# Performance work log

Measured on AMD Instinct MI355X. Metric: run time of the kernel, lower is better.

## Reference

```python
import jax, jax.numpy as jnp
import numpy as np

N = 50000          # nodes
E = 800000         # edges
F_IN = 128         # num_node_features
H = 64             # hidden_channels
G = 64             # graphs in batch
C = 10             # num_classes
L_HID = 3          # num_hidden_layers
EPS = 1e-5


def setup_inputs() -> dict:
    key = jax.random.key(0)
    ks = jax.random.split(key, 16)
    x = jax.random.normal(ks[0], (N, F_IN), dtype=jnp.float32)
    edge_index = jax.random.randint(ks[1], (2, E), 0, N, dtype=jnp.int32)
    batch = jnp.sort(jax.random.randint(ks[2], (N,), 0, G, dtype=jnp.int32))
    s = 0.05
    W_in = jax.random.normal(ks[3], (F_IN, H), dtype=jnp.float32) * s
    b_in = jnp.zeros((H,), dtype=jnp.float32)
    W_hid = jax.random.normal(ks[4], (L_HID, H, H), dtype=jnp.float32) * s
    b_hid = jnp.zeros((L_HID, H), dtype=jnp.float32)
    gamma = jnp.ones((H,), dtype=jnp.float32)
    beta = jnp.zeros((H,), dtype=jnp.float32)
    # MLPReadout: 64 -> 32 -> 16 -> 10
    W1 = jax.random.normal(ks[5], (H, H // 2), dtype=jnp.float32) * s
    b1 = jnp.zeros((H // 2,), dtype=jnp.float32)
    W2 = jax.random.normal(ks[6], (H // 2, H // 4), dtype=jnp.float32) * s
    b2 = jnp.zeros((H // 4,), dtype=jnp.float32)
    W3 = jax.random.normal(ks[7], (H // 4, C), dtype=jnp.float32) * s
    b3 = jnp.zeros((C,), dtype=jnp.float32)
    return {"x": x, "edge_index": edge_index, "batch": batch,
            "W_in": W_in, "b_in": b_in, "W_hid": W_hid, "b_hid": b_hid,
            "gamma": gamma, "beta": beta,
            "W1": W1, "b1": b1, "W2": W2, "b2": b2, "W3": W3, "b3": b3}


def gcn_conv(h_pre, W, b, src, dst, dis):
    # PyG GCNConv with self-loops: out_i = sum_{j->i} d_i^-.5 d_j^-.5 (x_j W) + d_i^-1 (x_i W) + b
    h = h_pre @ W                                   # [N, H]
    norm = (dis[src] * dis[dst])[:, None]           # [E, 1]
    agg = jax.ops.segment_sum(h[src] * norm, dst, num_segments=N)
    agg = agg + h * (dis * dis)[:, None]            # self-loop term
    return agg + b


def batchnorm(x, gamma, beta):
    mu = jnp.mean(x, axis=0)
    var = jnp.mean(jnp.square(x - mu), axis=0)      # biased var (torch BN)
    return (x - mu) * jax.lax.rsqrt(var + EPS) * gamma + beta


def reference(x, edge_index, batch, W_in, b_in, W_hid, b_hid,
              gamma, beta, W1, b1, W2, b2, W3, b3):
    src, dst = edge_index[0], edge_index[1]
    # degree with self-loops (computed on target nodes)
    deg = jax.ops.segment_sum(jnp.ones((E,), x.dtype), dst, num_segments=N) + 1.0
    dis = jax.lax.rsqrt(deg)                        # deg^-0.5

    h = jax.nn.relu(gcn_conv(x, W_in, b_in, src, dst, dis))
    for l in range(L_HID):
        h = gcn_conv(h, W_hid[l], b_hid[l], src, dst, dis)
        h = batchnorm(h, gamma, beta)
        h = jax.nn.relu(h)

    # global mean pool over graphs
    sums = jax.ops.segment_sum(h, batch, num_segments=G)           # [G, H]
    cnts = jax.ops.segment_sum(jnp.ones((N,), x.dtype), batch, num_segments=G)
    pooled = sums / jnp.maximum(cnts, 1.0)[:, None]

    # MLPReadout
    y = jax.nn.relu(pooled @ W1 + b1)
    y = jax.nn.relu(y @ W2 + b2)
    return y @ W3 + b3                               # [G, C]
```

## Files before the change

### kernel.cpp

```cpp
#include <hip/hip_runtime.h>

#define NN 50000
#define NE 800000
#define FIN 128
#define H 64
#define NG 64
#define NC 10
#define EPS 1e-5f
#define NB_SCAN 196
#define GATHER_BLOCKS 12500
#define BNRED_BLOCKS 125

__global__ void count_deg_kernel(const int* __restrict__ dst, int* __restrict__ deg) {
    int e = blockIdx.x * blockDim.x + threadIdx.x;
    if (e < NE) atomicAdd(&deg[dst[e]], 1);
}

__global__ void scan1_kernel(const int* __restrict__ deg, int* __restrict__ ebase,
                             int* __restrict__ bsum, float* __restrict__ dis) {
    __shared__ int s[256];
    int t = threadIdx.x;
    int i = blockIdx.x * 256 + t;
    int v = (i < NN) ? deg[i] : 0;
    if (i < NN) dis[i] = rsqrtf((float)v + 1.0f);
    s[t] = v;
    for (int off = 1; off < 256; off <<= 1) {
        __syncthreads();
        int add = (t >= off) ? s[t - off] : 0;
        __syncthreads();
        s[t] += add;
    }
    __syncthreads();
    if (i < NN) ebase[i] = s[t] - v;
    if (t == 255) bsum[blockIdx.x] = s[255];
}

__global__ void scan2_kernel(int* __restrict__ bsum, const int* __restrict__ batch,
                             int* __restrict__ gstart) {
    int t = threadIdx.x;
    if (t <= NG) {
        int lo = 0, hi = NN;
        while (lo < hi) {
            int mid = (lo + hi) >> 1;
            if (batch[mid] < t) lo = mid + 1; else hi = mid;
        }
        gstart[t] = lo;
    }
    __shared__ int s[256];
    int v = (t < NB_SCAN) ? bsum[t] : 0;
    s[t] = v;
    for (int off = 1; off < 256; off <<= 1) {
        __syncthreads();
        int add = (t >= off) ? s[t - off] : 0;
        __syncthreads();
        s[t] += add;
    }
    __syncthreads();
    if (t < NB_SCAN) bsum[t] = s[t] - v;
}

__global__ void scan3_kernel(int* __restrict__ ebase, const int* __restrict__ bsum) {
    int i = blockIdx.x * blockDim.x + threadIdx.x;
    if (i < NN) ebase[i] += bsum[i >> 8];
    if (i == 0) ebase[NN] = NE;
}

__global__ void fill_kernel(const int* __restrict__ src, const int* __restrict__ dst,
                            const int* __restrict__ ebase, int* __restrict__ cursor,
                            int* __restrict__ eidx) {
    int e = blockIdx.x * blockDim.x + threadIdx.x;
    if (e < NE) {
        int d = dst[e];
        int slot = ebase[d] + atomicAdd(&cursor[d], 1);
        eidx[slot] = src[e];
    }
}

__global__ __launch_bounds__(256, 4) void gemm_fin_kernel(const float* __restrict__ A,
                                                          const float* __restrict__ W,
                                                          const float* __restrict__ dis,
                                                          float* __restrict__ outp) {
    __shared__ float Al[64][65];
    __shared__ float Wl[64 * H];
    const int tid = threadIdx.x;
    const int r0 = blockIdx.x * 64;
    const int row = tid >> 2;
    const int cb  = (tid & 3) << 4;
    float acc[16];
#pragma unroll
    for (int j = 0; j < 16; j++) acc[j] = 0.f;

    for (int k0 = 0; k0 < FIN; k0 += 64) {
        for (int idx = tid; idx < 64 * H; idx += 256) Wl[idx] = W[k0 * H + idx];
        for (int idx = tid; idx < 64 * 64; idx += 256) {
            int r = idx >> 6, c = idx & 63;
            int gr = r0 + r;
            Al[r][c] = (gr < NN) ? A[(long)gr * FIN + k0 + c] : 0.f;
        }
        __syncthreads();
#pragma unroll
        for (int k = 0; k < 64; k++) {
            float a = Al[row][k];
#pragma unroll
            for (int j = 0; j < 16; j++) acc[j] = fmaf(a, Wl[k * H + cb + j], acc[j]);
        }
        __syncthreads();
    }
    int gr = r0 + row;
    if (gr < NN) {
        float ds = dis[gr];
#pragma unroll
        for (int j = 0; j < 16; j++) acc[j] *= ds;
        float4* o = reinterpret_cast<float4*>(&outp[(long)gr * H + cb]);
        o[0] = make_float4(acc[0], acc[1], acc[2], acc[3]);
        o[1] = make_float4(acc[4], acc[5], acc[6], acc[7]);
        o[2] = make_float4(acc[8], acc[9], acc[10], acc[11]);
        o[3] = make_float4(acc[12], acc[13], acc[14], acc[15]);
    }
}

template <int DO_BN>
__global__ __launch_bounds__(256, 4) void gemm_hid_kernel(const float* __restrict__ A,
                                                          const float* __restrict__ W,
                                                          const float* __restrict__ pbn2,
                                                          const float* __restrict__ gamma,
                                                          const float* __restrict__ beta,
                                                          const float* __restrict__ dis,
                                                          float* __restrict__ outp) {
    __shared__ float Al[64][65];
    __shared__ float Wl[64 * H];
    __shared__ float bns[128];
    __shared__ float tot[128];
    const int tid = threadIdx.x;
    if (DO_BN) {
        if (tid < 128) {
            float s = 0.f;
            for (int r = 0; r < BNRED_BLOCKS; ++r) s += pbn2[(long)r * 128 + tid];
            tot[tid] = s;
        }
        __syncthreads();
        if (tid < H) {
            float mu  = tot[tid] * (1.0f / NN);
            float var = tot[H + tid] * (1.0f / NN) - mu * mu;
            float sc  = rsqrtf(var + EPS) * gamma[tid];
            bns[tid]     = sc;
            bns[H + tid] = beta[tid] - mu * sc;
        }
        __syncthreads();
    }
    const int r0 = blockIdx.x * 64;
    const int row = tid >> 2;
    const int cb  = (tid & 3) << 4;
    float acc[16];
#pragma unroll
    for (int j = 0; j < 16; j++) acc[j] = 0.f;

    for (int idx = tid; idx < 64 * H; idx += 256) Wl[idx] = W[idx];
    for (int idx = tid; idx < 64 * 64; idx += 256) {
        int r = idx >> 6, c = idx & 63;
        int gr = r0 + r;
        float a = (gr < NN) ? A[(long)gr * H + c] : 0.f;
        if (DO_BN) a = fmaxf(fmaf(a, bns[c], bns[64 + c]), 0.f);
        Al[r][c] = a;
    }
    __syncthreads();
#pragma unroll
    for (int k = 0; k < 64; k++) {
        float a = Al[row][k];
#pragma unroll
        for (int j = 0; j < 16; j++) acc[j] = fmaf(a, Wl[k * H + cb + j], acc[j]);
    }
    int gr = r0 + row;
    if (gr < NN) {
        float ds = dis[gr];
#pragma unroll
        for (int j = 0; j < 16; j++) acc[j] *= ds;
        float4* o = reinterpret_cast<float4*>(&outp[(long)gr * H + cb]);
        o[0] = make_float4(acc[0], acc[1], acc[2], acc[3]);
        o[1] = make_float4(acc[4], acc[5], acc[6], acc[7]);
        o[2] = make_float4(acc[8], acc[9], acc[10], acc[11]);
        o[3] = make_float4(acc[12], acc[13], acc[14], acc[15]);
    }
}

template <int MODE>
__global__ __launch_bounds__(256) void gather_kernel(const float* __restrict__ hw,
                                                     const int* __restrict__ ebase,
                                                     const int* __restrict__ eidx,
                                                     const float* __restrict__ dis,
                                                     const float* __restrict__ bias,
                                                     float* __restrict__ outp,
                                                     float* __restrict__ pbn) {
    __shared__ float ls[H], lss[H];
    if (MODE == 1) {
        if (threadIdx.x < H) { ls[threadIdx.x] = 0.f; lss[threadIdx.x] = 0.f; }
        __syncthreads();
    }
    const int node = blockIdx.x * 4 + (threadIdx.x >> 6);
    const int lane = threadIdx.x & 63;
    const int grp  = lane >> 4;
    const int c4   = (lane & 15) << 2;
    const int e0 = ebase[node], e1 = ebase[node + 1];
    float4 acc = make_float4(0.f, 0.f, 0.f, 0.f);
    int e = e0 + grp;
    for (; e + 4 < e1; e += 8) {
        int s0 = eidx[e], s1 = eidx[e + 4];
        const float4 v0 = *reinterpret_cast<const float4*>(&hw[(long)s0 * H + c4]);
        const float4 v1 = *reinterpret_cast<const float4*>(&hw[(long)s1 * H + c4]);
        acc.x += v0.x + v1.x;
        acc.y += v0.y + v1.y;
        acc.z += v0.z + v1.z;
        acc.w += v0.w + v1.w;
    }
    if (e < e1) {
        const float4 v0 = *reinterpret_cast<const float4*>(&hw[(long)eidx[e] * H + c4]);
        acc.x += v0.x; acc.y += v0.y; acc.z += v0.z; acc.w += v0.w;
    }
#pragma unroll
    for (int m = 16; m <= 32; m <<= 1) {
        acc.x += __shfl_xor(acc.x, m, 64);
        acc.y += __shfl_xor(acc.y, m, 64);
        acc.z += __shfl_xor(acc.z, m, 64);
        acc.w += __shfl_xor(acc.w, m, 64);
    }
    const float4 self = *reinterpret_cast<const float4*>(&hw[(long)node * H + c4]);
    float ds = dis[node];
    float4 v;
    v.x = fmaf(acc.x + self.x, ds, bias[c4 + 0]);
    v.y = fmaf(acc.y + self.y, ds, bias[c4 + 1]);
    v.z = fmaf(acc.z + self.z, ds, bias[c4 + 2]);
    v.w = fmaf(acc.w + self.w, ds, bias[c4 + 3]);
    if (MODE == 0) {
        v.x = fmaxf(v.x, 0.f); v.y = fmaxf(v.y, 0.f);
        v.z = fmaxf(v.z, 0.f); v.w = fmaxf(v.w, 0.f);
    }
    if (grp == 0) {
        *reinterpret_cast<float4*>(&outp[(long)node * H + c4]) = v;
        if (MODE == 1) {
            atomicAdd(&ls[c4 + 0], v.x); atomicAdd(&lss[c4 + 0], v.x * v.x);
            atomicAdd(&ls[c4 + 1], v.y); atomicAdd(&lss[c4 + 1], v.y * v.y);
            atomicAdd(&ls[c4 + 2], v.z); atomicAdd(&lss[c4 + 2], v.z * v.z);
            atomicAdd(&ls[c4 + 3], v.w); atomicAdd(&lss[c4 + 3], v.w * v.w);
        }
    }
    if (MODE == 1) {
        __syncthreads();
        if (threadIdx.x < H) {
            pbn[(long)blockIdx.x * 128 + threadIdx.x] = ls[threadIdx.x];
            pbn[(long)blockIdx.x * 128 + H + threadIdx.x] = lss[threadIdx.x];
        }
    }
}

__global__ void bnredA_kernel(const float* __restrict__ pbn, float* __restrict__ pbn2) {
    int c = threadIdx.x & 127;
    int half = threadIdx.x >> 7;
    int r0 = blockIdx.x * 100;
    float s = 0.f;
    for (int r = r0 + half; r < r0 + 100; r += 2) s += pbn[(long)r * 128 + c];
    __shared__ float red[256];
    red[threadIdx.x] = s;
    __syncthreads();
    if (half == 0) pbn2[(long)blockIdx.x * 128 + c] = red[c] + red[128 + c];
}

__global__ void pool_mlp_kernel(const float* __restrict__ conv, const float* __restrict__ pbn2,
                                const float* __restrict__ gamma, const float* __restrict__ beta,
                                const int* __restrict__ gstart,
                                const float* __restrict__ W1, const float* __restrict__ b1,
                                const float* __restrict__ W2, const float* __restrict__ b2,
                                const float* __restrict__ W3, const float* __restrict__ b3,
                                float* __restrict__ out) {
    __shared__ float tot[128];
    __shared__ float bns[128];
    __shared__ float red[256];
    __shared__ float pl[H], y1[32], y2[16];
    const int t = threadIdx.x;
    const int g = blockIdx.x;
    if (t < 128) {
        float s = 0.f;
        for (int r = 0; r < BNRED_BLOCKS; ++r) s += pbn2[(long)r * 128 + t];
        tot[t] = s;
    }
    __syncthreads();
    if (t < H) {
        float mu  = tot[t] * (1.0f / NN);
        float var = tot[H + t] * (1.0f / NN) - mu * mu;
        float sc  = rsqrtf(var + EPS) * gamma[t];
        bns[t]     = sc;
        bns[H + t] = beta[t] - mu * sc;
    }
    __syncthreads();
    const int n0 = gstart[g], n1 = gstart[g + 1];
    const int sub = t >> 6, lane = t & 63;
    float sc = bns[lane], sh = bns[H + lane];
    float s = 0.f;
    for (int n = n0 + sub; n < n1; n += 4)
        s += fmaxf(fmaf(conv[(long)n * H + lane], sc, sh), 0.f);
    red[t] = s;
    __syncthreads();
    if (sub == 0) {
        float inv = 1.0f / fmaxf((float)(n1 - n0), 1.0f);
        pl[lane] = (red[lane] + red[64 + lane] + red[128 + lane] + red[192 + lane]) * inv;
    }
    __syncthreads();
    if (t < 32) {
        float v = b1[t];
        for (int k = 0; k < H; k++) v = fmaf(pl[k], W1[k * 32 + t], v);
        y1[t] = fmaxf(v, 0.f);
    }
    __syncthreads();
    if (t < 16) {
        float v = b2[t];
        for (int k = 0; k < 32; k++) v = fmaf(y1[k], W2[k * 16 + t], v);
        y2[t] = fmaxf(v, 0.f);
    }
    __syncthreads();
    if (t < NC) {
        float v = b3[t];
        for (int k = 0; k < 16; k++) v = fmaf(y2[k], W3[k * NC + t], v);
        out[(long)g * NC + t] = v;
    }
}

extern "C" void kernel_launch(void* const* d_in, const int* in_sizes, int n_in,
                              void* d_out, int out_size, void* d_ws, size_t ws_size,
                              hipStream_t stream) {
    const float* x     = (const float*)d_in[0];
    const int*   ei    = (const int*)d_in[1];
    const int*   batch = (const int*)d_in[2];
    const float* W_in  = (const float*)d_in[3];
    const float* b_in  = (const float*)d_in[4];
    const float* W_hid = (const float*)d_in[5];
    const float* b_hid = (const float*)d_in[6];
    const float* gamma = (const float*)d_in[7];
    const float* beta  = (const float*)d_in[8];
    const float* W1    = (const float*)d_in[9];
    const float* b1    = (const float*)d_in[10];
    const float* W2    = (const float*)d_in[11];
    const float* b2    = (const float*)d_in[12];
    const float* W3    = (const float*)d_in[13];
    const float* b3    = (const float*)d_in[14];
    float* out = (float*)d_out;

    const int* src = ei;
    const int* dst = ei + NE;

    int*   deg_i  = (int*)d_ws;
    int*   cursor = deg_i + 50048;
    int*   ebase  = cursor + 50048;
    int*   eidx   = ebase + 50056;
    int*   bsum   = eidx + 800000;
    int*   gstart = bsum + 256;
    float* dis    = (float*)(gstart + 72);
    float* hw     = dis + 50048;
    float* conv   = hw + (long)NN * H;
    float* h      = conv + (long)NN * H;
    float* pbn    = h + (long)NN * H;
    float* pbn2   = pbn + (long)GATHER_BLOCKS * 128;

    const int NB_GEMM = (NN + 63) / 64;
    const int NB_E    = (NE + 255) / 256;
    const int NB_N    = (NN + 255) / 256;

    hipMemsetAsync(deg_i, 0, 2 * 50048 * sizeof(int), stream);
    count_deg_kernel<<<NB_E, 256, 0, stream>>>(dst, deg_i);
    scan1_kernel<<<NB_SCAN, 256, 0, stream>>>(deg_i, ebase, bsum, dis);
    scan2_kernel<<<1, 256, 0, stream>>>(bsum, batch, gstart);
    scan3_kernel<<<NB_N, 256, 0, stream>>>(ebase, bsum);
    fill_kernel<<<NB_E, 256, 0, stream>>>(src, dst, ebase, cursor, eidx);

    gemm_fin_kernel<<<NB_GEMM, 256, 0, stream>>>(x, W_in, dis, hw);
    gather_kernel<0><<<GATHER_BLOCKS, 256, 0, stream>>>(hw, ebase, eidx, dis, b_in, h, nullptr);

    gemm_hid_kernel<0><<<NB_GEMM, 256, 0, stream>>>(h, W_hid, nullptr, nullptr, nullptr, dis, hw);
    gather_kernel<1><<<GATHER_BLOCKS, 256, 0, stream>>>(hw, ebase, eidx, dis, b_hid, conv, pbn);
    bnredA_kernel<<<BNRED_BLOCKS, 256, 0, stream>>>(pbn, pbn2);
    for (int l = 1; l < 3; l++) {
        gemm_hid_kernel<1><<<NB_GEMM, 256, 0, stream>>>(conv, W_hid + (long)l * H * H, pbn2,
                                                        gamma, beta, dis, hw);
        gather_kernel<1><<<GATHER_BLOCKS, 256, 0, stream>>>(hw, ebase, eidx, dis,
                                                            b_hid + (long)l * H, conv, pbn);
        bnredA_kernel<<<BNRED_BLOCKS, 256, 0, stream>>>(pbn, pbn2);
    }

    pool_mlp_kernel<<<NG, 256, 0, stream>>>(conv, pbn2, gamma, beta, gstart,
                                            W1, b1, W2, b2, W3, b3, out);
}
```

Measured before the change: 609.7 us.

## Split node features into 8-column slabs for cache-friendly gather, split BN/pool reductions

GEMM outputs are now written in a column-grouped layout of eight 8-float slabs, each NN×8. The gather kernel launches eight times as many blocks, and each block aggregates one slab, so each slab's random gather working set (1.6MB) can stay cache-resident. The BN statistics finalisation moves out of every GEMM block into a single-block bnredB kernel. Pooling is split into a parallel partial-sum kernel plus a small MLP kernel. The trade-off is more launches, 32-byte scattered reads per edge, and eight passes over the edge index lists.

Result: slower. 790.8 us (+29.7%).

```diff
diff --git a/kernel.cpp b/kernel.cpp
--- a/kernel.cpp
+++ b/kernel.cpp
@@ -9,6 +9,7 @@
 #define EPS 1e-5f
 #define NB_SCAN 196
 #define GATHER_BLOCKS 12500
+#define NGRP 8
 #define BNRED_BLOCKS 125
 
 __global__ void count_deg_kernel(const int* __restrict__ dst, int* __restrict__ deg) {
@@ -79,7 +80,7 @@
 __global__ __launch_bounds__(256, 4) void gemm_fin_kernel(const float* __restrict__ A,
                                                           const float* __restrict__ W,
                                                           const float* __restrict__ dis,
-                                                          float* __restrict__ outp) {
+                                                          float* __restrict__ hwt) {
     __shared__ float Al[64][65];
     __shared__ float Wl[64 * H];
     const int tid = threadIdx.x;
@@ -111,41 +112,28 @@
         float ds = dis[gr];
 #pragma unroll
         for (int j = 0; j < 16; j++) acc[j] *= ds;
-        float4* o = reinterpret_cast<float4*>(&outp[(long)gr * H + cb]);
-        o[0] = make_float4(acc[0], acc[1], acc[2], acc[3]);
-        o[1] = make_float4(acc[4], acc[5], acc[6], acc[7]);
-        o[2] = make_float4(acc[8], acc[9], acc[10], acc[11]);
-        o[3] = make_float4(acc[12], acc[13], acc[14], acc[15]);
+        int g0 = cb >> 3;
+        float4* p0 = reinterpret_cast<float4*>(&hwt[((long)g0 * NN + gr) * 8]);
+        p0[0] = make_float4(acc[0], acc[1], acc[2], acc[3]);
+        p0[1] = make_float4(acc[4], acc[5], acc[6], acc[7]);
+        float4* p1 = reinterpret_cast<float4*>(&hwt[((long)(g0 + 1) * NN + gr) * 8]);
+        p1[0] = make_float4(acc[8], acc[9], acc[10], acc[11]);
+        p1[1] = make_float4(acc[12], acc[13], acc[14], acc[15]);
     }
 }
 
 template <int DO_BN>
 __global__ __launch_bounds__(256, 4) void gemm_hid_kernel(const float* __restrict__ A,
                                                           const float* __restrict__ W,
-                                                          const float* __restrict__ pbn2,
-                                                          const float* __restrict__ gamma,
-                                                          const float* __restrict__ beta,
+                                                          const float* __restrict__ bnsc,
                                                           const float* __restrict__ dis,
-                                                          float* __restrict__ outp) {
+                                                          float* __restrict__ hwt) {
     __shared__ float Al[64][65];
     __shared__ float Wl[64 * H];
     __shared__ float bns[128];
-    __shared__ float tot[128];
     const int tid = threadIdx.x;
     if (DO_BN) {
-        if (tid < 128) {
-            float s = 0.f;
-            for (int r = 0; r < BNRED_BLOCKS; ++r) s += pbn2[(long)r * 128 + tid];
-            tot[tid] = s;
-        }
-        __syncthreads();
-        if (tid < H) {
-            float mu  = tot[tid] * (1.0f / NN);
-            float var = tot[H + tid] * (1.0f / NN) - mu * mu;
-            float sc  = rsqrtf(var + EPS) * gamma[tid];
-            bns[tid]     = sc;
-            bns[H + tid] = beta[tid] - mu * sc;
-        }
+        if (tid < 128) bns[tid] = bnsc[tid];
         __syncthreads();
     }
     const int r0 = blockIdx.x * 64;
@@ -175,79 +163,60 @@
         float ds = dis[gr];
 #pragma unroll
         for (int j = 0; j < 16; j++) acc[j] *= ds;
-        float4* o = reinterpret_cast<float4*>(&outp[(long)gr * H + cb]);
-        o[0] = make_float4(acc[0], acc[1], acc[2], acc[3]);
-        o[1] = make_float4(acc[4], acc[5], acc[6], acc[7]);
-        o[2] = make_float4(acc[8], acc[9], acc[10], acc[11]);
-        o[3] = make_float4(acc[12], acc[13], acc[14], acc[15]);
+        int g0 = cb >> 3;
+        float4* p0 = reinterpret_cast<float4*>(&hwt[((long)g0 * NN + gr) * 8]);
+        p0[0] = make_float4(acc[0], acc[1], acc[2], acc[3]);
+        p0[1] = make_float4(acc[4], acc[5], acc[6], acc[7]);
+        float4* p1 = reinterpret_cast<float4*>(&hwt[((long)(g0 + 1) * NN + gr) * 8]);
+        p1[0] = make_float4(acc[8], acc[9], acc[10], acc[11]);
+        p1[1] = make_float4(acc[12], acc[13], acc[14], acc[15]);
     }
 }
 
 template <int MODE>
-__global__ __launch_bounds__(256) void gather_kernel(const float* __restrict__ hw,
+__global__ __launch_bounds__(256) void gather_kernel(const float* __restrict__ hwt,
                                                      const int* __restrict__ ebase,
                                                      const int* __restrict__ eidx,
                                                      const float* __restrict__ dis,
                                                      const float* __restrict__ bias,
                                                      float* __restrict__ outp,
                                                      float* __restrict__ pbn) {
-    __shared__ float ls[H], lss[H];
+    __shared__ float ls[8], lss[8];
+    const int b = blockIdx.x;
+    const int grp = b & (NGRP - 1);
+    const int nb  = b >> 3;
+    const int t = threadIdx.x;
     if (MODE == 1) {
-        if (threadIdx.x < H) { ls[threadIdx.x] = 0.f; lss[threadIdx.x] = 0.f; }
-        __syncthreads();
-    }
-    const int node = blockIdx.x * 4 + (threadIdx.x >> 6);
-    const int lane = threadIdx.x & 63;
-    const int grp  = lane >> 4;
-    const int c4   = (lane & 15) << 2;
+        if (t < 8) { ls[t] = 0.f; lss[t] = 0.f; }
+        __syncthreads();
+    }
+    const int node = nb * 4 + (t >> 6);
+    const int lane = t & 63;
+    const int eoff = lane >> 3;
+    const int c    = lane & 7;
+    const float* __restrict__ tab = hwt + (long)grp * NN * 8;
     const int e0 = ebase[node], e1 = ebase[node + 1];
-    float4 acc = make_float4(0.f, 0.f, 0.f, 0.f);
-    int e = e0 + grp;
-    for (; e + 4 < e1; e += 8) {
-        int s0 = eidx[e], s1 = eidx[e + 4];
-        const float4 v0 = *reinterpret_cast<const float4*>(&hw[(long)s0 * H + c4]);
-        const float4 v1 = *reinterpret_cast<const float4*>(&hw[(long)s1 * H + c4]);
-        acc.x += v0.x + v1.x;
-        acc.y += v0.y + v1.y;
-        acc.z += v0.z + v1.z;
-        acc.w += v0.w + v1.w;
-    }
-    if (e < e1) {
-        const float4 v0 = *reinterpret_cast<const float4*>(&hw[(long)eidx[e] * H + c4]);
-        acc.x += v0.x; acc.y += v0.y; acc.z += v0.z; acc.w += v0.w;
-    }
-#pragma unroll
-    for (int m = 16; m <= 32; m <<= 1) {
-        acc.x += __shfl_xor(acc.x, m, 64);
-        acc.y += __shfl_xor(acc.y, m, 64);
-        acc.z += __shfl_xor(acc.z, m, 64);
-        acc.w += __shfl_xor(acc.w, m, 64);
-    }
-    const float4 self = *reinterpret_cast<const float4*>(&hw[(long)node * H + c4]);
-    float ds = dis[node];
-    float4 v;
-    v.x = fmaf(acc.x + self.x, ds, bias[c4 + 0]);
-    v.y = fmaf(acc.y + self.y, ds, bias[c4 + 1]);
-    v.z = fmaf(acc.z + self.z, ds, bias[c4 + 2]);
-    v.w = fmaf(acc.w + self.w, ds, bias[c4 + 3]);
-    if (MODE == 0) {
-        v.x = fmaxf(v.x, 0.f); v.y = fmaxf(v.y, 0.f);
-        v.z = fmaxf(v.z, 0.f); v.w = fmaxf(v.w, 0.f);
-    }
-    if (grp == 0) {
-        *reinterpret_cast<float4*>(&outp[(long)node * H + c4]) = v;
+    float acc = 0.f;
+    for (int e = e0 + eoff; e < e1; e += 8)
+        acc += tab[(long)eidx[e] * 8 + c];
+    acc += __shfl_xor(acc, 8, 64);
+    acc += __shfl_xor(acc, 16, 64);
+    acc += __shfl_xor(acc, 32, 64);
+    if (eoff == 0) {
+        float self = tab[(long)node * 8 + c];
+        float v = fmaf(acc + self, dis[node], bias[grp * 8 + c]);
+        if (MODE == 0) v = fmaxf(v, 0.f);
+        outp[(long)node * H + grp * 8 + c] = v;
         if (MODE == 1) {
-            atomicAdd(&ls[c4 + 0], v.x); atomicAdd(&lss[c4 + 0], v.x * v.x);
-            atomicAdd(&ls[c4 + 1], v.y); atomicAdd(&lss[c4 + 1], v.y * v.y);
-            atomicAdd(&ls[c4 + 2], v.z); atomicAdd(&lss[c4 + 2], v.z * v.z);
-            atomicAdd(&ls[c4 + 3], v.w); atomicAdd(&lss[c4 + 3], v.w * v.w);
+            atomicAdd(&ls[c], v);
+            atomicAdd(&lss[c], v * v);
         }
     }
     if (MODE == 1) {
         __syncthreads();
-        if (threadIdx.x < H) {
-            pbn[(long)blockIdx.x * 128 + threadIdx.x] = ls[threadIdx.x];
-            pbn[(long)blockIdx.x * 128 + H + threadIdx.x] = lss[threadIdx.x];
+        if (t < 8) {
+            pbn[(long)nb * 128 + grp * 8 + t] = ls[t];
+            pbn[(long)nb * 128 + 64 + grp * 8 + t] = lss[t];
         }
     }
 }
@@ -264,45 +233,53 @@
     if (half == 0) pbn2[(long)blockIdx.x * 128 + c] = red[c] + red[128 + c];
 }
 
-__global__ void pool_mlp_kernel(const float* __restrict__ conv, const float* __restrict__ pbn2,
-                                const float* __restrict__ gamma, const float* __restrict__ beta,
-                                const int* __restrict__ gstart,
-                                const float* __restrict__ W1, const float* __restrict__ b1,
-                                const float* __restrict__ W2, const float* __restrict__ b2,
-                                const float* __restrict__ W3, const float* __restrict__ b3,
-                                float* __restrict__ out) {
+__global__ void bnredB_kernel(const float* __restrict__ pbn2, const float* __restrict__ gamma,
+                              const float* __restrict__ beta, float* __restrict__ bnsc) {
     __shared__ float tot[128];
-    __shared__ float bns[128];
-    __shared__ float red[256];
-    __shared__ float pl[H], y1[32], y2[16];
-    const int t = threadIdx.x;
-    const int g = blockIdx.x;
-    if (t < 128) {
-        float s = 0.f;
-        for (int r = 0; r < BNRED_BLOCKS; ++r) s += pbn2[(long)r * 128 + t];
-        tot[t] = s;
-    }
+    int t = threadIdx.x;
+    float s = 0.f;
+    for (int r = 0; r < BNRED_BLOCKS; ++r) s += pbn2[(long)r * 128 + t];
+    tot[t] = s;
     __syncthreads();
     if (t < H) {
         float mu  = tot[t] * (1.0f / NN);
         float var = tot[H + t] * (1.0f / NN) - mu * mu;
         float sc  = rsqrtf(var + EPS) * gamma[t];
-        bns[t]     = sc;
-        bns[H + t] = beta[t] - mu * sc;
-    }
-    __syncthreads();
+        bnsc[t]     = sc;
+        bnsc[H + t] = beta[t] - mu * sc;
+    }
+}
+
+__global__ __launch_bounds__(256) void poolA_kernel(const float* __restrict__ conv,
+                                                    const float* __restrict__ bnsc,
+                                                    const int* __restrict__ gstart,
+                                                    float* __restrict__ psum) {
+    const int g = blockIdx.x >> 3, s = blockIdx.x & 7;
     const int n0 = gstart[g], n1 = gstart[g + 1];
-    const int sub = t >> 6, lane = t & 63;
-    float sc = bns[lane], sh = bns[H + lane];
+    const int wave = threadIdx.x >> 6, lane = threadIdx.x & 63;
+    const float sc = bnsc[lane], sh = bnsc[H + lane];
+    float acc = 0.f;
+    for (int n = n0 + s + 8 * wave; n < n1; n += 32)
+        acc += fmaxf(fmaf(conv[(long)n * H + lane], sc, sh), 0.f);
+    __shared__ float red[256];
+    red[threadIdx.x] = acc;
+    __syncthreads();
+    if (wave == 0)
+        psum[(long)blockIdx.x * H + lane] = red[lane] + red[64 + lane] + red[128 + lane] + red[192 + lane];
+}
+
+__global__ void poolB_mlp_kernel(const float* __restrict__ psum, const int* __restrict__ gstart,
+                                 const float* __restrict__ W1, const float* __restrict__ b1,
+                                 const float* __restrict__ W2, const float* __restrict__ b2,
+                                 const float* __restrict__ W3, const float* __restrict__ b3,
+                                 float* __restrict__ out) {
+    __shared__ float pl[H], y1[32], y2[16];
+    const int g = blockIdx.x, t = threadIdx.x;
     float s = 0.f;
-    for (int n = n0 + sub; n < n1; n += 4)
-        s += fmaxf(fmaf(conv[(long)n * H + lane], sc, sh), 0.f);
-    red[t] = s;
-    __syncthreads();
-    if (sub == 0) {
-        float inv = 1.0f / fmaxf((float)(n1 - n0), 1.0f);
-        pl[lane] = (red[lane] + red[64 + lane] + red[128 + lane] + red[192 + lane]) * inv;
-    }
+#pragma unroll
+    for (int k = 0; k < 8; k++) s += psum[(long)(g * 8 + k) * H + t];
+    const int n0 = gstart[g], n1 = gstart[g + 1];
+    pl[t] = s / fmaxf((float)(n1 - n0), 1.0f);
     __syncthreads();
     if (t < 32) {
         float v = b1[t];
@@ -353,15 +330,18 @@
     int*   bsum   = eidx + 800000;
     int*   gstart = bsum + 256;
     float* dis    = (float*)(gstart + 72);
-    float* hw     = dis + 50048;
-    float* conv   = hw + (long)NN * H;
+    float* hwt    = dis + 50048;
+    float* conv   = hwt + (long)NN * H;
     float* h      = conv + (long)NN * H;
     float* pbn    = h + (long)NN * H;
     float* pbn2   = pbn + (long)GATHER_BLOCKS * 128;
+    float* bnsc   = pbn2 + BNRED_BLOCKS * 128;
+    float* psum   = bnsc + 128;
 
     const int NB_GEMM = (NN + 63) / 64;
     const int NB_E    = (NE + 255) / 256;
     const int NB_N    = (NN + 255) / 256;
+    const int NB_GATH = GATHER_BLOCKS * NGRP;
 
     hipMemsetAsync(deg_i, 0, 2 * 50048 * sizeof(int), stream);
     count_deg_kernel<<<NB_E, 256, 0, stream>>>(dst, deg_i);
@@ -370,20 +350,21 @@
     scan3_kernel<<<NB_N, 256, 0, stream>>>(ebase, bsum);
     fill_kernel<<<NB_E, 256, 0, stream>>>(src, dst, ebase, cursor, eidx);
 
-    gemm_fin_kernel<<<NB_GEMM, 256, 0, stream>>>(x, W_in, dis, hw);
-    gather_kernel<0><<<GATHER_BLOCKS, 256, 0, stream>>>(hw, ebase, eidx, dis, b_in, h, nullptr);
-
-    gemm_hid_kernel<0><<<NB_GEMM, 256, 0, stream>>>(h, W_hid, nullptr, nullptr, nullptr, dis, hw);
-    gather_kernel<1><<<GATHER_BLOCKS, 256, 0, stream>>>(hw, ebase, eidx, dis, b_hid, conv, pbn);
+    gemm_fin_kernel<<<NB_GEMM, 256, 0, stream>>>(x, W_in, dis, hwt);
+    gather_kernel<0><<<NB_GATH, 256, 0, stream>>>(hwt, ebase, eidx, dis, b_in, h, nullptr);
+
+    gemm_hid_kernel<0><<<NB_GEMM, 256, 0, stream>>>(h, W_hid, nullptr, dis, hwt);
+    gather_kernel<1><<<NB_GATH, 256, 0, stream>>>(hwt, ebase, eidx, dis, b_hid, conv, pbn);
     bnredA_kernel<<<BNRED_BLOCKS, 256, 0, stream>>>(pbn, pbn2);
+    bnredB_kernel<<<1, 128, 0, stream>>>(pbn2, gamma, beta, bnsc);
     for (int l = 1; l < 3; l++) {
-        gemm_hid_kernel<1><<<NB_GEMM, 256, 0, stream>>>(conv, W_hid + (long)l * H * H, pbn2,
-                                                        gamma, beta, dis, hw);
-        gather_kernel<1><<<GATHER_BLOCKS, 256, 0, stream>>>(hw, ebase, eidx, dis,
-                                                            b_hid + (long)l * H, conv, pbn);
+        gemm_hid_kernel<1><<<NB_GEMM, 256, 0, stream>>>(conv, W_hid + (long)l * H * H, bnsc, dis, hwt);
+        gather_kernel<1><<<NB_GATH, 256, 0, stream>>>(hwt, ebase, eidx, dis,
+                                                      b_hid + (long)l * H, conv, pbn);
         bnredA_kernel<<<BNRED_BLOCKS, 256, 0, stream>>>(pbn, pbn2);
-    }
-
-    pool_mlp_kernel<<<NG, 256, 0, stream>>>(conv, pbn2, gamma, beta, gstart,
-                                            W1, b1, W2, b2, W3, b3, out);
-}
+        bnredB_kernel<<<1, 128, 0, stream>>>(pbn2, gamma, beta, bnsc);
+    }
+
+    poolA_kernel<<<NG * 8, 256, 0, stream>>>(conv, bnsc, gstart, psum);
+    poolB_mlp_kernel<<<NG, 64, 0, stream>>>(psum, gstart, W1, b1, W2, b2, W3, b3, out);
+}
```
